# Kernel tuning notes

Measured on AMD Instinct MI355X. Metric: run time of the kernel, lower is better.

Reference implementation:

```python
import jax, jax.numpy as jnp
import numpy as np

H = 16          # nhead
N_LAYERS = 4    # stacks (weights are SHARED across stacks, as in the torch module)
PAD_IDX = 1
EPS = 1e-6
NEG = -1e9


def _pos_encoding(S, d):
    den = jnp.exp(-jnp.arange(0, d, 2, dtype=jnp.float32) * (np.log(10000.0) / d))
    ang = jnp.arange(S, dtype=jnp.float32)[:, None] * den[None, :]  # (S, d/2)
    pe = jnp.zeros((S, d), jnp.float32)
    pe = pe.at[:, 0::2].set(jnp.sin(ang)).at[:, 1::2].set(jnp.cos(ang))
    return pe


def _layer_norm(x, g, b):
    mu = jnp.mean(x, axis=-1, keepdims=True)
    var = jnp.mean((x - mu) ** 2, axis=-1, keepdims=True)
    return (x - mu) * jax.lax.rsqrt(var + EPS) * g + b


def _split_heads(x):
    B, S, d = x.shape
    return x.reshape(B, S, H, d // H).transpose(0, 2, 1, 3)  # (B,H,S,dk)


def _mha(q_in, k_in, v_in, mask, wq, bq, wk, bk, wv, bv, wo, bo):
    q = _split_heads(q_in @ wq + bq)
    k = _split_heads(k_in @ wk + bk)
    v = _split_heads(v_in @ wv + bv)
    dk = v.shape[-1]
    score = jnp.einsum('bhqd,bhkd->bhqk', q, k) / jnp.sqrt(jnp.float32(dk))
    if mask is not None:
        score = jnp.where(mask, score, NEG)
    p = jax.nn.softmax(score, axis=-1)
    out = jnp.einsum('bhqk,bhkd->bhqd', p, v)
    B, _, S, _ = out.shape
    out = out.transpose(0, 2, 1, 3).reshape(B, S, H * dk)
    return out @ wo + bo


def setup_inputs() -> dict:
    key = jax.random.key(0)
    B, St, Sm, d, dff, V = 4, 1024, 1024, 1024, 4096, 32000
    ks = jax.random.split(key, 32)
    sc = 1.0 / np.sqrt(d)
    inp = {
        'target_result': jax.random.randint(ks[0], (B, St), 0, V),
        'memory': jax.random.normal(ks[1], (B, Sm, d), jnp.float32),
        'emb': jax.random.normal(ks[2], (V, d), jnp.float32) * sc,
        'ff_w1': jax.random.normal(ks[3], (d, dff), jnp.float32) * sc,
        'ff_b1': jnp.zeros((dff,), jnp.float32),
        'ff_w2': jax.random.normal(ks[4], (dff, d), jnp.float32) / np.sqrt(dff),
        'ff_b2': jnp.zeros((d,), jnp.float32),
        'ln_g': jnp.ones((d,), jnp.float32),
        'ln_b': jnp.zeros((d,), jnp.float32),
    }
    i = 5
    for pre in ('sa', 'xa'):
        for nm in ('q', 'k', 'v', 'o'):
            inp[f'{pre}_w{nm}'] = jax.random.normal(ks[i], (d, d), jnp.float32) * sc
            inp[f'{pre}_b{nm}'] = jnp.zeros((d,), jnp.float32)
            i += 1
    return inp


def reference(target_result, memory, emb,
              sa_wq, sa_bq, sa_wk, sa_bk, sa_wv, sa_bv, sa_wo, sa_bo,
              xa_wq, xa_bq, xa_wk, xa_bk, xa_wv, xa_bv, xa_wo, xa_bo,
              ff_w1, ff_b1, ff_w2, ff_b2, ln_g, ln_b):
    B, St = target_result.shape
    d = emb.shape[1]
    # embed + scale + positional encoding (dropout = eval/identity)
    x = emb[target_result] * jnp.sqrt(jnp.float32(d)) + _pos_encoding(St, d)[None]
    # masks: pad mask (B,1,St,1) & causal (St,St) -> (B,1,St,St); source mask all-ones -> None
    pad = (target_result != PAD_IDX)[:, None, :, None]
    causal = jnp.tril(jnp.ones((St, St), bool))[None, None]
    tgt_mask = pad & causal
    out = x
    for _ in range(N_LAYERS):
        n = _layer_norm(out, ln_g, ln_b)
        out = out + _mha(n, n, n, tgt_mask,
                         sa_wq, sa_bq, sa_wk, sa_bk, sa_wv, sa_bv, sa_wo, sa_bo)
        n = _layer_norm(out, ln_g, ln_b)
        out = out + _mha(n, memory, memory, None,
                         xa_wq, xa_bq, xa_wk, xa_bk, xa_wv, xa_bv, xa_wo, xa_bo)
        n = _layer_norm(out, ln_g, ln_b)
        out = out + (jax.nn.relu(n @ ff_w1 + ff_b1) @ ff_w2 + ff_b2)
    return _layer_norm(out, ln_g, ln_b)
```

## Files before the change

kernel.cpp:

```cpp
#include <hip/hip_runtime.h>

typedef unsigned short u16;
typedef unsigned int u32;
typedef float f32x4 __attribute__((ext_vector_type(4)));
typedef float f32x16 __attribute__((ext_vector_type(16)));
typedef __bf16 bf16x8 __attribute__((ext_vector_type(8)));
typedef short short8 __attribute__((ext_vector_type(8)));
typedef u32 u32x4 __attribute__((ext_vector_type(4)));

#define DINLINE static __device__ __forceinline__

DINLINE u16 f2bf(float f) {
  u32 u = __builtin_bit_cast(u32, f);
  u += 0x7fffu + ((u >> 16) & 1u);
  return (u16)(u >> 16);
}

DINLINE float b2f(u32 lo16) {
  u32 u = lo16 << 16;
  return __builtin_bit_cast(float, u);
}

DINLINE f32x4 mfma16(short8 a, short8 b, f32x4 c) {
  return __builtin_amdgcn_mfma_f32_16x16x32_bf16(
      __builtin_bit_cast(bf16x8, a), __builtin_bit_cast(bf16x8, b), c, 0, 0, 0);
}

DINLINE f32x16 mfma32(short8 a, short8 b, f32x16 c) {
  return __builtin_amdgcn_mfma_f32_32x32x16_bf16(
      __builtin_bit_cast(bf16x8, a), __builtin_bit_cast(bf16x8, b), c, 0, 0, 0);
}

DINLINE u32 cvtpk(float lo, float hi) {
  u32 r;
  asm("v_cvt_pk_bf16_f32 %0, %1, %2" : "=v"(r) : "v"(lo), "v"(hi));
  return r;
}

DINLINE void plswap(u32& a, u32& b) {
  auto r = __builtin_amdgcn_permlane32_swap(a, b, false, false);
  a = (u32)r[0];
  b = (u32)r[1];
}

DINLINE void gld16(const void* g, void* l) {
  __builtin_amdgcn_global_load_lds(
      (const __attribute__((address_space(1))) void*)g,
      (__attribute__((address_space(3))) void*)l, 16, 0, 0);
}

__global__ __launch_bounds__(256) void transpose_wt(const float* __restrict__ src,
                                                    u16* __restrict__ dst, int K, int N,
                                                    float scale) {
  __shared__ float tile[32][33];
  int n0 = blockIdx.x * 32, k0 = blockIdx.y * 32;
  int tx = threadIdx.x, ty = threadIdx.y;
#pragma unroll
  for (int j = 0; j < 32; j += 8)
    tile[ty + j][tx] = src[(size_t)(k0 + ty + j) * N + n0 + tx];
  __syncthreads();
#pragma unroll
  for (int j = 0; j < 32; j += 8)
    dst[(size_t)(n0 + ty + j) * K + k0 + tx] = f2bf(tile[tx][ty + j] * scale);
}

__global__ __launch_bounds__(256) void cvt_bf16(const float* __restrict__ src,
                                                u16* __restrict__ dst) {
  size_t i = (size_t)blockIdx.x * 256 + threadIdx.x;
  float4 v = ((const float4*)src)[i];
  u32 lo = (u32)f2bf(v.x) | ((u32)f2bf(v.y) << 16);
  u32 hi = (u32)f2bf(v.z) | ((u32)f2bf(v.w) << 16);
  uint2 o; o.x = lo; o.y = hi;
  ((uint2*)dst)[i] = o;
}

__global__ void concat3(const float* __restrict__ a, const float* __restrict__ b,
                        const float* __restrict__ c, float* __restrict__ o, float sa) {
  int i = blockIdx.x * 256 + threadIdx.x;
  float v = (i < 1024) ? a[i] * sa : (i < 2048 ? b[i - 1024] : c[i - 2048]);
  o[i] = v;
}

__global__ void scale_vec(const float* __restrict__ a, float* __restrict__ o, float s) {
  int i = blockIdx.x * 256 + threadIdx.x;
  o[i] = a[i] * s;
}

__global__ __launch_bounds__(256) void pe_k(float* __restrict__ pe) {
  int s = blockIdx.x;
  for (int c = threadIdx.x; c < 1024; c += 256) {
    int i = c >> 1;
    float den = expf(-(float)(2 * i) * 0.0089944739960705f);
    float ang = (float)s * den;
    pe[s * 1024 + c] = (c & 1) ? cosf(ang) : sinf(ang);
  }
}

__global__ __launch_bounds__(256) void embed_pe(const int* __restrict__ tgt,
                                                const float* __restrict__ emb,
                                                const float* __restrict__ pe,
                                                float* __restrict__ x,
                                                u16* __restrict__ xbf) {
  int row = blockIdx.x;
  int s = row & 1023;
  int tok = tgt[row];
  float4 e = ((const float4*)(emb + (size_t)tok * 1024))[threadIdx.x];
  float4 p = ((const float4*)(pe + (size_t)s * 1024))[threadIdx.x];
  float4 o;
  o.x = e.x * 32.0f + p.x; o.y = e.y * 32.0f + p.y;
  o.z = e.z * 32.0f + p.z; o.w = e.w * 32.0f + p.w;
  ((float4*)(x + (size_t)row * 1024))[threadIdx.x] = o;
  ushort4 ob;
  ob.x = f2bf(o.x); ob.y = f2bf(o.y); ob.z = f2bf(o.z); ob.w = f2bf(o.w);
  ((ushort4*)(xbf + (size_t)row * 1024))[threadIdx.x] = ob;
}

template <int MODE>
__global__ __launch_bounds__(256) void ln2_k(const float* __restrict__ Xf,
                                             const u16* __restrict__ Xb,
                                             const float* __restrict__ g,
                                             const float* __restrict__ bta,
                                             u16* __restrict__ obf,
                                             float* __restrict__ of) {
  const int t = threadIdx.x;
  const int row = blockIdx.x * 2 + (t >> 7);
  const int c = t & 127;
  float v[8];
  if (MODE == 1) {
    float4 a = ((const float4*)(Xf + (size_t)row * 1024))[c * 2];
    float4 b4 = ((const float4*)(Xf + (size_t)row * 1024))[c * 2 + 1];
    v[0] = a.x; v[1] = a.y; v[2] = a.z; v[3] = a.w;
    v[4] = b4.x; v[5] = b4.y; v[6] = b4.z; v[7] = b4.w;
  } else {
    u32x4 p = *(const u32x4*)(Xb + (size_t)row * 1024 + c * 8);
#pragma unroll
    for (int i = 0; i < 4; ++i) {
      v[2 * i] = b2f(p[i]);
      v[2 * i + 1] = b2f(p[i] >> 16);
    }
  }
  float s = 0.f, sq = 0.f;
#pragma unroll
  for (int i = 0; i < 8; ++i) { s += v[i]; sq += v[i] * v[i]; }
#pragma unroll
  for (int o = 1; o < 64; o <<= 1) {
    s += __shfl_xor(s, o);
    sq += __shfl_xor(sq, o);
  }
  __shared__ float red[8];
  const int wid = t >> 6;
  if ((t & 63) == 0) { red[wid * 2] = s; red[wid * 2 + 1] = sq; }
  __syncthreads();
  const int base = (t >> 7) * 4;
  s = red[base] + red[base + 2];
  sq = red[base + 1] + red[base + 3];
  float mean = s * (1.0f / 1024.0f);
  float var = sq * (1.0f / 1024.0f) - mean * mean;
  float rstd = rsqrtf(var + 1e-6f);
  float4 g0 = ((const float4*)g)[c * 2], g1 = ((const float4*)g)[c * 2 + 1];
  float4 b0 = ((const float4*)bta)[c * 2], b1 = ((const float4*)bta)[c * 2 + 1];
  float gv[8] = {g0.x, g0.y, g0.z, g0.w, g1.x, g1.y, g1.z, g1.w};
  float bv[8] = {b0.x, b0.y, b0.z, b0.w, b1.x, b1.y, b1.z, b1.w};
  float y[8];
#pragma unroll
  for (int i = 0; i < 8; ++i) y[i] = (v[i] - mean) * rstd * gv[i] + bv[i];
  if (MODE == 1) {
    float4 o0, o1;
    o0.x = y[0]; o0.y = y[1]; o0.z = y[2]; o0.w = y[3];
    o1.x = y[4]; o1.y = y[5]; o1.z = y[6]; o1.w = y[7];
    ((float4*)(of + (size_t)row * 1024))[c * 2] = o0;
    ((float4*)(of + (size_t)row * 1024))[c * 2 + 1] = o1;
  } else {
    u32x4 o;
#pragma unroll
    for (int i = 0; i < 4; ++i)
      o[i] = (u32)f2bf(y[2 * i]) | ((u32)f2bf(y[2 * i + 1]) << 16);
    *(u32x4*)(obf + (size_t)row * 1024 + c * 8) = o;
  }
}

template <int BM, int EPI>
__global__ __launch_bounds__(256) void gemm2(
    const u16* __restrict__ A, const u16* __restrict__ Bt,
    const float* __restrict__ bias, float* __restrict__ X,
    u16* __restrict__ Cbf, int N, int K) {
  constexpr int ABYT = BM * 128;
  constexpr int BBYT = 128 * 128;
  constexpr int MF = BM / 32;
  __shared__ __align__(16) char smem[2 * (ABYT + BBYT)];

  const int tid = threadIdx.x;
  const int w = tid >> 6, l = tid & 63;
  const int lg = l >> 4, lc = l & 15;
  const int nwg = gridDim.x * gridDim.y;
  int bid = blockIdx.y * gridDim.x + blockIdx.x;
  bid = (bid & 7) * (nwg >> 3) + (bid >> 3);
  const int m0 = (bid / gridDim.x) * BM, n0 = (bid % gridDim.x) * 128;
  const int wr = w >> 1, wc = w & 1;
  const char* Ab = (const char*)A;
  const char* Bb = (const char*)Bt;
  const size_t sA = (size_t)K * 2;

  f32x4 acc[MF][4];
  const f32x4 zv = {0.f, 0.f, 0.f, 0.f};
#pragma unroll
  for (int m = 0; m < MF; ++m)
#pragma unroll
    for (int n = 0; n < 4; ++n) acc[m][n] = zv;

  const int srow = l >> 3;
  const int scol = ((l & 7) ^ srow) << 4;

  auto stage = [&](char* bufA, char* bufB, int kt) {
    const size_t kb = (size_t)kt << 7;
#pragma unroll
    for (int i = 0; i < BM / 32; ++i) {
      const int r = i * 32 + w * 8 + srow;
      gld16(Ab + (size_t)(m0 + r) * sA + kb + scol, bufA + (i * 4 + w) * 1024 + l * 16);
    }
#pragma unroll
    for (int i = 0; i < 4; ++i) {
      const int r = i * 32 + w * 8 + srow;
      gld16(Bb + (size_t)(n0 + r) * sA + kb + scol, bufB + (i * 4 + w) * 1024 + l * 16);
    }
  };

  stage(smem, smem + ABYT, 0);
  __syncthreads();

  const int nkt = K >> 6;
  int cur = 0;
  for (int kt = 0; kt < nkt; ++kt) {
    char* As = smem + cur * (ABYT + BBYT);
    char* Bs = As + ABYT;
    if (kt + 1 < nkt) {
      char* An = smem + (cur ^ 1) * (ABYT + BBYT);
      stage(An, An + ABYT, kt + 1);
    }
    __builtin_amdgcn_s_setprio(1);
#pragma unroll
    for (int ks = 0; ks < 2; ++ks) {
      short8 af[MF], bf4[4];
#pragma unroll
      for (int m = 0; m < MF; ++m) {
        int row = wr * (BM / 2) + m * 16 + lc;
        int col = (ks * 64 + (lg << 4)) ^ ((row & 7) << 4);
        af[m] = *(const short8*)(As + row * 128 + col);
      }
#pragma unroll
      for (int n = 0; n < 4; ++n) {
        int row = wc * 64 + n * 16 + lc;
        int col = (ks * 64 + (lg << 4)) ^ ((row & 7) << 4);
        bf4[n] = *(const short8*)(Bs + row * 128 + col);
      }
#pragma unroll
      for (int m = 0; m < MF; ++m)
#pragma unroll
        for (int n = 0; n < 4; ++n) acc[m][n] = mfma16(af[m], bf4[n], acc[m][n]);
    }
    __builtin_amdgcn_s_setprio(0);
    __syncthreads();
    cur ^= 1;
  }

  float bv[4];
#pragma unroll
  for (int n = 0; n < 4; ++n) bv[n] = bias[n0 + wc * 64 + n * 16 + lc];

  if (EPI <= 1) {
    u16* ct = (u16*)smem;
#pragma unroll
    for (int m = 0; m < MF; ++m)
#pragma unroll
      for (int n = 0; n < 4; ++n)
#pragma unroll
        for (int r = 0; r < 4; ++r) {
          int row = wr * (BM / 2) + m * 16 + (lg << 2) + r;
          int col = wc * 64 + n * 16 + lc;
          float v = acc[m][n][r] + bv[n];
          if (EPI == 1) v = v > 0.f ? v : 0.f;
          ct[row * 136 + col] = f2bf(v);
        }
    __syncthreads();
#pragma unroll
    for (int j = 0; j < BM / 16; ++j) {
      int c = j * 256 + tid;
      int row = c >> 4, colb = (c & 15) * 8;
      *(short8*)(Cbf + (size_t)(m0 + row) * N + n0 + colb) =
          *(const short8*)(ct + row * 136 + colb);
    }
  } else if (EPI == 2) {
    float* cf = (float*)smem;
#pragma unroll
    for (int m = 0; m < MF; ++m)
#pragma unroll
      for (int n = 0; n < 4; ++n)
#pragma unroll
        for (int r = 0; r < 4; ++r) {
          int row = wr * (BM / 2) + m * 16 + (lg << 2) + r;
          int col = wc * 64 + n * 16 + lc;
          cf[row * 128 + col] = acc[m][n][r] + bv[n];
        }
    __syncthreads();
#pragma unroll
    for (int j = 0; j < BM / 8; ++j) {
      int c = j * 256 + tid;
      int row = c >> 5, colb = (c & 31) * 4;
      size_t idx = (size_t)(m0 + row) * N + n0 + colb;
      float4 s4 = *(const float4*)(cf + row * 128 + colb);
      float4 xv = *(const float4*)(X + idx);
      xv.x += s4.x; xv.y += s4.y; xv.z += s4.z; xv.w += s4.w;
      *(float4*)(X + idx) = xv;
      ushort4 ob;
      ob.x = f2bf(xv.x); ob.y = f2bf(xv.y); ob.z = f2bf(xv.z); ob.w = f2bf(xv.w);
      *(ushort4*)(Cbf + idx) = ob;
    }
  } else {
    u16* ct = (u16*)smem;
#pragma unroll
    for (int m = 0; m < MF; ++m)
#pragma unroll
      for (int n = 0; n < 4; ++n)
#pragma unroll
        for (int r = 0; r < 4; ++r) {
          int row = wr * (BM / 2) + m * 16 + (lg << 2) + r;
          int col = wc * 64 + n * 16 + lc;
          ct[col * 136 + row] = f2bf(acc[m][n][r] + bv[n]);
        }
    __syncthreads();
    const int bb = m0 >> 10, ms = m0 & 1023;
#pragma unroll
    for (int j = 0; j < BM / 16; ++j) {
      int flat = j * 256 + tid;
      int sb = flat & (BM / 8 - 1);
      int col = flat / (BM / 8);
      int n = n0 + col;
      u16* dst = Cbf + (size_t)(((bb << 4) + (n >> 6)) * 64 + (n & 63)) * 1024 + ms + sb * 8;
      *(short8*)dst = *(const short8*)(ct + col * 136 + sb * 8);
    }
  }
}

template <int BM, int EPI>
__global__ __launch_bounds__(256) void gemm2c(
    const u16* __restrict__ A, const u16* __restrict__ Bt,
    const float* __restrict__ bias, float* __restrict__ X,
    u16* __restrict__ Cbf, int N, int K) {
  constexpr int ABYT = BM * 128;
  constexpr int BBYT = 128 * 128;
  constexpr int BUF = ABYT + BBYT;
  constexpr int MF = BM / 32;
  __shared__ __align__(16) char smem[3 * BUF];

  const int tid = threadIdx.x;
  const int w = tid >> 6, l = tid & 63;
  const int lg = l >> 4, lc = l & 15;
  const int nwg = gridDim.x * gridDim.y;
  int bid = blockIdx.y * gridDim.x + blockIdx.x;
  bid = (bid & 7) * (nwg >> 3) + (bid >> 3);
  const int m0 = (bid / gridDim.x) * BM, n0 = (bid % gridDim.x) * 128;
  const int wr = w >> 1, wc = w & 1;
  const char* Ab = (const char*)A;
  const char* Bb = (const char*)Bt;
  const size_t sA = (size_t)K * 2;

  f32x4 acc[MF][4];
  const f32x4 zv = {0.f, 0.f, 0.f, 0.f};
#pragma unroll
  for (int m = 0; m < MF; ++m)
#pragma unroll
    for (int n = 0; n < 4; ++n) acc[m][n] = zv;

  const int srow = l >> 3;
  const int scol = ((l & 7) ^ srow) << 4;

  auto stage = [&](char* buf, int kt) {
    const size_t kb = (size_t)kt << 7;
#pragma unroll
    for (int i = 0; i < BM / 32; ++i) {
      const int r = i * 32 + w * 8 + srow;
      gld16(Ab + (size_t)(m0 + r) * sA + kb + scol, buf + (i * 4 + w) * 1024 + l * 16);
    }
#pragma unroll
    for (int i = 0; i < 4; ++i) {
      const int r = i * 32 + w * 8 + srow;
      gld16(Bb + (size_t)(n0 + r) * sA + kb + scol,
            buf + ABYT + (i * 4 + w) * 1024 + l * 16);
    }
  };

  char* p0 = smem;
  char* p1 = smem + BUF;
  char* p2 = smem + 2 * BUF;

  stage(p0, 0);
  stage(p1, 1);
  __builtin_amdgcn_sched_barrier(0);
  asm volatile("s_waitcnt vmcnt(6)" ::: "memory");
  __builtin_amdgcn_s_barrier();
  __builtin_amdgcn_sched_barrier(0);

  const int nkt = K >> 6;
  for (int kt = 0; kt < nkt; ++kt) {
    if (kt + 2 < nkt) stage(p2, kt + 2);
    const char* As = p0;
    const char* Bs = p0 + ABYT;
    __builtin_amdgcn_s_setprio(1);
#pragma unroll
    for (int ks = 0; ks < 2; ++ks) {
      short8 af[MF], bf4[4];
#pragma unroll
      for (int m = 0; m < MF; ++m) {
        int row = wr * (BM / 2) + m * 16 + lc;
        int col = (ks * 64 + (lg << 4)) ^ ((row & 7) << 4);
        af[m] = *(const short8*)(As + row * 128 + col);
      }
#pragma unroll
      for (int n = 0; n < 4; ++n) {
        int row = wc * 64 + n * 16 + lc;
        int col = (ks * 64 + (lg << 4)) ^ ((row & 7) << 4);
        bf4[n] = *(const short8*)(Bs + row * 128 + col);
      }
#pragma unroll
      for (int m = 0; m < MF; ++m)
#pragma unroll
        for (int n = 0; n < 4; ++n) acc[m][n] = mfma16(af[m], bf4[n], acc[m][n]);
    }
    __builtin_amdgcn_s_setprio(0);
    __builtin_amdgcn_sched_barrier(0);
    if (kt + 2 < nkt) {
      asm volatile("s_waitcnt vmcnt(6) lgkmcnt(0)" ::: "memory");
    } else {
      asm volatile("s_waitcnt vmcnt(0) lgkmcnt(0)" ::: "memory");
    }
    __builtin_amdgcn_s_barrier();
    __builtin_amdgcn_sched_barrier(0);
    char* t = p0; p0 = p1; p1 = p2; p2 = t;
  }

  float bv[4];
#pragma unroll
  for (int n = 0; n < 4; ++n) bv[n] = bias[n0 + wc * 64 + n * 16 + lc];

  if (EPI <= 1) {
    u16* ct = (u16*)smem;
#pragma unroll
    for (int m = 0; m < MF; ++m)
#pragma unroll
      for (int n = 0; n < 4; ++n)
#pragma unroll
        for (int r = 0; r < 4; ++r) {
          int row = wr * (BM / 2) + m * 16 + (lg << 2) + r;
          int col = wc * 64 + n * 16 + lc;
          float v = acc[m][n][r] + bv[n];
          if (EPI == 1) v = v > 0.f ? v : 0.f;
          ct[row * 136 + col] = f2bf(v);
        }
    __syncthreads();
#pragma unroll
    for (int j = 0; j < BM / 16; ++j) {
      int c = j * 256 + tid;
      int row = c >> 4, colb = (c & 15) * 8;
      *(short8*)(Cbf + (size_t)(m0 + row) * N + n0 + colb) =
          *(const short8*)(ct + row * 136 + colb);
    }
  } else if (EPI == 2) {
    float* cf = (float*)smem;
#pragma unroll
    for (int m = 0; m < MF; ++m)
#pragma unroll
      for (int n = 0; n < 4; ++n)
#pragma unroll
        for (int r = 0; r < 4; ++r) {
          int row = wr * (BM / 2) + m * 16 + (lg << 2) + r;
          int col = wc * 64 + n * 16 + lc;
          cf[row * 128 + col] = acc[m][n][r] + bv[n];
        }
    __syncthreads();
#pragma unroll
    for (int j = 0; j < BM / 8; ++j) {
      int c = j * 256 + tid;
      int row = c >> 5, colb = (c & 31) * 4;
      size_t idx = (size_t)(m0 + row) * N + n0 + colb;
      float4 s4 = *(const float4*)(cf + row * 128 + colb);
      float4 xv = *(const float4*)(X + idx);
      xv.x += s4.x; xv.y += s4.y; xv.z += s4.z; xv.w += s4.w;
      *(float4*)(X + idx) = xv;
      ushort4 ob;
      ob.x = f2bf(xv.x); ob.y = f2bf(xv.y); ob.z = f2bf(xv.z); ob.w = f2bf(xv.w);
      *(ushort4*)(Cbf + idx) = ob;
    }
  } else {
    u16* ct = (u16*)smem;
#pragma unroll
    for (int m = 0; m < MF; ++m)
#pragma unroll
      for (int n = 0; n < 4; ++n)
#pragma unroll
        for (int r = 0; r < 4; ++r) {
          int row = wr * (BM / 2) + m * 16 + (lg << 2) + r;
          int col = wc * 64 + n * 16 + lc;
          ct[col * 136 + row] = f2bf(acc[m][n][r] + bv[n]);
        }
    __syncthreads();
    const int bb = m0 >> 10, ms = m0 & 1023;
#pragma unroll
    for (int j = 0; j < BM / 16; ++j) {
      int flat = j * 256 + tid;
      int sb = flat & (BM / 8 - 1);
      int col = flat / (BM / 8);
      int n = n0 + col;
      u16* dst = Cbf + (size_t)(((bb << 4) + (n >> 6)) * 64 + (n & 63)) * 1024 + ms + sb * 8;
      *(short8*)dst = *(const short8*)(ct + col * 136 + sb * 8);
    }
  }
}

template <bool CAUSAL>
__global__ __launch_bounds__(256) void attn_lds(
    const u16* __restrict__ Qp, int sQ, const u16* __restrict__ Kp, int sK,
    const u16* __restrict__ Vt, const int* __restrict__ tgt,
    u16* __restrict__ Out) {
  __shared__ __align__(16) char smem[2][32768];
  const int tid = threadIdx.x;
  const int w = tid >> 6, l = tid & 63;
  const int bh = blockIdx.x & 63;
  const int p = blockIdx.x >> 6;
  const int sub = CAUSAL ? ((p < 4) ? p : 11 - p) : p;
  const int b = bh >> 4, h = bh & 15;
  const int lq = l & 31, hi = l >> 5;
  const int qt = sub * 4 + w;
  const int q0 = qt * 32;

  const char* Kc = (const char*)(Kp + (size_t)b * 1024 * sK + h * 64);
  const char* Vc = (const char*)(Vt + (size_t)bh * 64 * 1024);
  const u16* Qh = Qp + (size_t)b * 1024 * sQ + h * 64;

  short8 qb[4];
  {
    const u16* qrow = Qh + (size_t)(q0 + lq) * sQ + hi * 8;
#pragma unroll
    for (int c = 0; c < 4; ++c) qb[c] = *(const short8*)(qrow + c * 16);
  }

  bool row_ok = true;
  int my_nkt = 16;
  int blk_nst = CAUSAL ? (sub + 1) : 8;
  if (CAUSAL) {
    row_ok = (tgt[b * 1024 + q0 + lq] != 1);
    bool anypad_w = __any(!row_ok);
    __shared__ int s_pad;
    if (tid == 0) s_pad = 0;
    __syncthreads();
    if (anypad_w && l == 0) s_pad = 1;
    __syncthreads();
    if (s_pad) { my_nkt = 16; blk_nst = 8; }
    else my_nkt = (qt >> 1) + 1;
  }

  const int srow = l >> 3;
  const int scol = ((l & 7) ^ srow) << 4;
  auto stage = [&](int buf, int st) {
    const int k0 = st * 128;
    char* Ks = smem[buf];
    char* Vs = smem[buf] + 16384;
#pragma unroll
    for (int t2 = 0; t2 < 2; ++t2)
#pragma unroll
      for (int i = 0; i < 2; ++i) {
        const int r = i * 32 + w * 8 + srow;
        gld16(Kc + (size_t)(k0 + t2 * 64 + r) * sK * 2 + scol, Ks + t2 * 8192 + r * 128);
        gld16(Vc + (size_t)r * 2048 + (size_t)(k0 + t2 * 64) * 2 + scol,
              Vs + t2 * 8192 + r * 128);
      }
  };

  float m = -3.0e38f, lsum = 0.f;
  f32x16 oacc[2];
#pragma unroll
  for (int r = 0; r < 16; ++r) { oacc[0][r] = 0.f; oacc[1][r] = 0.f; }

  stage(0, 0);
  __syncthreads();
  int cur = 0;

  for (int st = 0; st < blk_nst; ++st) {
    if (st + 1 < blk_nst) stage(cur ^ 1, st + 1);
#pragma unroll
    for (int t2 = 0; t2 < 2; ++t2) {
      const int t64 = st * 2 + t2;
      if (t64 < my_nkt) {
        const char* Ks = smem[cur] + t2 * 8192;
        const char* Vs = smem[cur] + 16384 + t2 * 8192;
        const int k0 = t64 * 64;
        f32x16 stt[2];
        __builtin_amdgcn_s_setprio(1);
#pragma unroll
        for (int s = 0; s < 2; ++s) {
          const int row = s * 32 + lq;
          const int swz = (row & 7) << 4;
          f32x16 a;
#pragma unroll
          for (int r = 0; r < 16; ++r) a[r] = 0.f;
#pragma unroll
          for (int c = 0; c < 4; ++c) {
            short8 kb = *(const short8*)(Ks + row * 128 + ((c * 32 + hi * 16) ^ swz));
            a = mfma32(kb, qb[c], a);
          }
          stt[s] = a;
        }
        __builtin_amdgcn_s_setprio(0);
        if (CAUSAL) {
#pragma unroll
          for (int s = 0; s < 2; ++s) {
            if (!row_ok || (k0 + s * 32 + 31 > q0)) {
#pragma unroll
              for (int r = 0; r < 16; ++r) {
                int kg = k0 + s * 32 + (r & 3) + 8 * (r >> 2) + 4 * hi;
                bool ok = row_ok && (kg <= q0 + lq);
                if (!ok) stt[s][r] = -1e9f;
              }
            }
          }
        }
        float tm;
        {
          float v[16];
#pragma unroll
          for (int r = 0; r < 16; ++r) v[r] = fmaxf(stt[0][r], stt[1][r]);
#pragma unroll
          for (int w2 = 8; w2 >= 1; w2 >>= 1)
#pragma unroll
            for (int r = 0; r < w2; ++r) v[r] = fmaxf(v[r], v[r + w2]);
          tm = v[0];
        }
        tm = fmaxf(tm, __shfl_xor(tm, 32));
        if (!__all(tm <= m + 8.0f)) {
          float mn = fmaxf(m, tm);
          float alpha = __expf(m - mn);
          lsum *= alpha;
          m = mn;
#pragma unroll
          for (int r = 0; r < 16; ++r) {
            int crow = (r & 3) + 8 * (r >> 2) + 4 * hi;
            float av = __shfl(alpha, crow);
            oacc[0][r] *= av;
            oacc[1][r] *= av;
          }
        }
        float tsa0 = 0.f, tsa1 = 0.f, tsa2 = 0.f, tsa3 = 0.f;
#pragma unroll
        for (int s = 0; s < 2; ++s) {
#pragma unroll
          for (int r = 0; r < 16; ++r) {
            float e = __expf(stt[s][r] - m);
            stt[s][r] = e;
            if ((r & 3) == 0) tsa0 += e;
            else if ((r & 3) == 1) tsa1 += e;
            else if ((r & 3) == 2) tsa2 += e;
            else tsa3 += e;
          }
        }
        float ts = (tsa0 + tsa1) + (tsa2 + tsa3);
        ts += __shfl_xor(ts, 32);
        lsum += ts;
        short8 pa[4];
#pragma unroll
        for (int s = 0; s < 2; ++s) {
          u32 cc[8];
#pragma unroll
          for (int t = 0; t < 4; ++t) {
            cc[2 * t]     = cvtpk(stt[s][4 * t + 0], stt[s][4 * t + 1]);
            cc[2 * t + 1] = cvtpk(stt[s][4 * t + 2], stt[s][4 * t + 3]);
          }
          plswap(cc[0], cc[2]);
          plswap(cc[1], cc[3]);
          plswap(cc[4], cc[6]);
          plswap(cc[5], cc[7]);
          u32x4 w0 = {cc[0], cc[1], cc[2], cc[3]};
          u32x4 w1 = {cc[4], cc[5], cc[6], cc[7]};
          pa[2 * s]     = __builtin_bit_cast(short8, w0);
          pa[2 * s + 1] = __builtin_bit_cast(short8, w1);
        }
        __builtin_amdgcn_s_setprio(1);
#pragma unroll
        for (int dt = 0; dt < 2; ++dt) {
          const int row = dt * 32 + lq;
          const int swz = (row & 7) << 4;
#pragma unroll
          for (int c = 0; c < 4; ++c) {
            short8 vb = *(const short8*)(Vs + row * 128 + ((c * 32 + hi * 16) ^ swz));
            oacc[dt] = mfma32(pa[c], vb, oacc[dt]);
          }
        }
        __builtin_amdgcn_s_setprio(0);
      }
    }
    __syncthreads();
    cur ^= 1;
  }

#pragma unroll
  for (int r = 0; r < 16; ++r) {
    int crow = (r & 3) + 8 * (r >> 2) + 4 * hi;
    float lv = __shfl(lsum, crow);
    float linv = 1.0f / lv;
    int qg = q0 + crow;
    size_t base = ((size_t)b * 1024 + qg) * 1024 + h * 64 + lq;
    Out[base] = f2bf(oacc[0][r] * linv);
    Out[base + 32] = f2bf(oacc[1][r] * linv);
  }
}

extern "C" void kernel_launch(void* const* d_in, const int* in_sizes, int n_in,
                              void* d_out, int out_size, void* d_ws, size_t ws_size,
                              hipStream_t stream) {
  const int* tgt = (const int*)d_in[0];
  const float* memory = (const float*)d_in[1];
  const float* emb = (const float*)d_in[2];
  const float* ff_w1 = (const float*)d_in[3];
  const float* ff_b1 = (const float*)d_in[4];
  const float* ff_w2 = (const float*)d_in[5];
  const float* ff_b2 = (const float*)d_in[6];
  const float* ln_g = (const float*)d_in[7];
  const float* ln_b = (const float*)d_in[8];
  const float* sa_wq = (const float*)d_in[9];
  const float* sa_bq = (const float*)d_in[10];
  const float* sa_wk = (const float*)d_in[11];
  const float* sa_bk = (const float*)d_in[12];
  const float* sa_wv = (const float*)d_in[13];
  const float* sa_bv = (const float*)d_in[14];
  const float* sa_wo = (const float*)d_in[15];
  const float* sa_bo = (const float*)d_in[16];
  const float* xa_wq = (const float*)d_in[17];
  const float* xa_bq = (const float*)d_in[18];
  const float* xa_wk = (const float*)d_in[19];
  const float* xa_bk = (const float*)d_in[20];
  const float* xa_wv = (const float*)d_in[21];
  const float* xa_bv = (const float*)d_in[22];
  const float* xa_wo = (const float*)d_in[23];
  const float* xa_bo = (const float*)d_in[24];

  char* ws = (char*)d_ws;
  size_t off = 0;
  auto alloc = [&](size_t bytes) {
    char* p = ws + off;
    off += (bytes + 255) & ~(size_t)255;
    return p;
  };
  float* x   = (float*)alloc(4096ull * 1024 * 4);
  u16* xbf   = (u16*)alloc(4096ull * 1024 * 2);
  u16* nbf   = (u16*)alloc(4096ull * 1024 * 2);
  u16* qkv   = (u16*)alloc(4096ull * 2048 * 2);
  u16* q2    = (u16*)alloc(4096ull * 1024 * 2);
  u16* attn  = (u16*)alloc(4096ull * 1024 * 2);
  u16* vt    = (u16*)alloc(64ull * 64 * 1024 * 2);
  u16* kx    = (u16*)alloc(4096ull * 1024 * 2);
  u16* vtx   = (u16*)alloc(64ull * 64 * 1024 * 2);
  u16* h1    = (u16*)alloc(4096ull * 4096 * 2);
  u16* memb  = (u16*)alloc(4096ull * 1024 * 2);
  u16* w_qkv = (u16*)alloc(3072ull * 1024 * 2);
  u16* w_sao = (u16*)alloc(1024ull * 1024 * 2);
  u16* w_xaq = (u16*)alloc(1024ull * 1024 * 2);
  u16* w_xak = (u16*)alloc(1024ull * 1024 * 2);
  u16* w_xav = (u16*)alloc(1024ull * 1024 * 2);
  u16* w_xao = (u16*)alloc(1024ull * 1024 * 2);
  u16* w_ff1 = (u16*)alloc(4096ull * 1024 * 2);
  u16* w_ff2 = (u16*)alloc(1024ull * 4096 * 2);
  float* b_qkv = (float*)alloc(3072 * 4);
  float* b_xaq = (float*)alloc(1024 * 4);
  float* pe    = (float*)alloc(1024ull * 1024 * 4);

  dim3 blk(256);
  dim3 b32(32, 8);
  const float QS = 0.125f;

  transpose_wt<<<dim3(32, 32), b32, 0, stream>>>(sa_wq, w_qkv, 1024, 1024, QS);
  transpose_wt<<<dim3(32, 32), b32, 0, stream>>>(sa_wk, w_qkv + 1024 * 1024, 1024, 1024, 1.f);
  transpose_wt<<<dim3(32, 32), b32, 0, stream>>>(sa_wv, w_qkv + 2048 * 1024, 1024, 1024, 1.f);
  transpose_wt<<<dim3(32, 32), b32, 0, stream>>>(sa_wo, w_sao, 1024, 1024, 1.f);
  transpose_wt<<<dim3(32, 32), b32, 0, stream>>>(xa_wq, w_xaq, 1024, 1024, QS);
  transpose_wt<<<dim3(32, 32), b32, 0, stream>>>(xa_wk, w_xak, 1024, 1024, 1.f);
  transpose_wt<<<dim3(32, 32), b32, 0, stream>>>(xa_wv, w_xav, 1024, 1024, 1.f);
  transpose_wt<<<dim3(32, 32), b32, 0, stream>>>(xa_wo, w_xao, 1024, 1024, 1.f);
  transpose_wt<<<dim3(128, 32), b32, 0, stream>>>(ff_w1, w_ff1, 1024, 4096, 1.f);
  transpose_wt<<<dim3(32, 128), b32, 0, stream>>>(ff_w2, w_ff2, 4096, 1024, 1.f);
  concat3<<<12, blk, 0, stream>>>(sa_bq, sa_bk, sa_bv, b_qkv, QS);
  scale_vec<<<4, blk, 0, stream>>>(xa_bq, b_xaq, QS);
  cvt_bf16<<<4096, blk, 0, stream>>>(memory, memb);
  pe_k<<<1024, blk, 0, stream>>>(pe);
  embed_pe<<<4096, blk, 0, stream>>>(tgt, emb, pe, x, xbf);

  gemm2c<64, 0><<<dim3(8, 64), blk, 0, stream>>>(memb, w_xak, xa_bk, nullptr, kx, 1024, 1024);
  gemm2c<64, 3><<<dim3(8, 64), blk, 0, stream>>>(memb, w_xav, xa_bv, nullptr, vtx, 1024, 1024);

  for (int layer = 0; layer < 4; ++layer) {
    ln2_k<2><<<2048, blk, 0, stream>>>(nullptr, xbf, ln_g, ln_b, nbf, nullptr);
    gemm2<128, 0><<<dim3(16, 32), blk, 0, stream>>>(nbf, w_qkv, b_qkv, nullptr, qkv, 2048, 1024);
    gemm2c<64, 3><<<dim3(8, 64), blk, 0, stream>>>(nbf, w_qkv + 2048 * 1024, b_qkv + 2048,
                                                   nullptr, vt, 1024, 1024);
    attn_lds<true><<<512, blk, 0, stream>>>(qkv, 2048, qkv + 1024, 2048, vt, tgt, attn);
    gemm2c<64, 2><<<dim3(8, 64), blk, 0, stream>>>(attn, w_sao, sa_bo, x, xbf, 1024, 1024);
    ln2_k<2><<<2048, blk, 0, stream>>>(nullptr, xbf, ln_g, ln_b, nbf, nullptr);
    gemm2c<64, 0><<<dim3(8, 64), blk, 0, stream>>>(nbf, w_xaq, b_xaq, nullptr, q2, 1024, 1024);
    attn_lds<false><<<512, blk, 0, stream>>>(q2, 1024, kx, 1024, vtx, nullptr, attn);
    gemm2c<64, 2><<<dim3(8, 64), blk, 0, stream>>>(attn, w_xao, xa_bo, x, xbf, 1024, 1024);
    ln2_k<2><<<2048, blk, 0, stream>>>(nullptr, xbf, ln_g, ln_b, nbf, nullptr);
    gemm2<128, 1><<<dim3(32, 32), blk, 0, stream>>>(nbf, w_ff1, ff_b1, nullptr, h1, 4096, 1024);
    gemm2c<64, 2><<<dim3(8, 64), blk, 0, stream>>>(h1, w_ff2, ff_b2, x, xbf, 1024, 4096);
  }
  ln2_k<1><<<2048, blk, 0, stream>>>(x, nullptr, ln_g, ln_b, nullptr, (float*)d_out);
}
```

Measured before the change: 1.082 ms.

## Fold LayerNorm into GEMMs via gamma-scaled weights and epilogue row-stat correction

Removes the standalone LayerNorm kernels inside the layer loop. Gamma is folded into the transposed weights, and the beta and bias terms go into precomputed column vectors u and c. The consumer GEMMs read the raw bf16 residual and apply per-row rstd and mean corrections in the epilogue. The residual-add GEMM epilogues (and the embedding kernel) write per-tile partial row sums and sums of squares, which the next GEMM reduces into the row statistics. This saves a full read/write pass of the activations three times per layer, at the cost of extra epilogue work. It also changes numerics: the mean-subtraction now happens after a bf16 matmul on the uncentred input (E[x²]-μ² cancellation), and the statistics come from fp32 values rather than the bf16 copy.

```diff
diff --git a/kernel.cpp b/kernel.cpp
--- a/kernel.cpp
+++ b/kernel.cpp
@@ -62,6 +62,39 @@
 #pragma unroll
   for (int j = 0; j < 32; j += 8)
     dst[(size_t)(n0 + ty + j) * K + k0 + tx] = f2bf(tile[tx][ty + j] * scale);
+}
+
+__global__ __launch_bounds__(256) void transpose_wtg(const float* __restrict__ src,
+                                                     u16* __restrict__ dst, int K, int N,
+                                                     float scale, const float* __restrict__ g) {
+  __shared__ float tile[32][33];
+  int n0 = blockIdx.x * 32, k0 = blockIdx.y * 32;
+  int tx = threadIdx.x, ty = threadIdx.y;
+#pragma unroll
+  for (int j = 0; j < 32; j += 8)
+    tile[ty + j][tx] = src[(size_t)(k0 + ty + j) * N + n0 + tx];
+  __syncthreads();
+  float gk = g[k0 + tx] * scale;
+#pragma unroll
+  for (int j = 0; j < 32; j += 8)
+    dst[(size_t)(n0 + ty + j) * K + k0 + tx] = f2bf(tile[tx][ty + j] * gk);
+}
+
+__global__ __launch_bounds__(256) void ucol_k(const float* __restrict__ g,
+                                              const float* __restrict__ bln,
+                                              const float* __restrict__ W,
+                                              const float* __restrict__ bias,
+                                              float scale, int N,
+                                              float* __restrict__ u, float* __restrict__ c) {
+  int n = blockIdx.x * 256 + threadIdx.x;
+  float us = 0.f, cs = 0.f;
+  for (int k = 0; k < 1024; ++k) {
+    float wv = W[(size_t)k * N + n];
+    us += g[k] * wv;
+    cs += bln[k] * wv;
+  }
+  u[n] = scale * us;
+  c[n] = scale * (cs + bias[n]);
 }
 
 __global__ __launch_bounds__(256) void cvt_bf16(const float* __restrict__ src,
@@ -74,18 +107,6 @@
   ((uint2*)dst)[i] = o;
 }
 
-__global__ void concat3(const float* __restrict__ a, const float* __restrict__ b,
-                        const float* __restrict__ c, float* __restrict__ o, float sa) {
-  int i = blockIdx.x * 256 + threadIdx.x;
-  float v = (i < 1024) ? a[i] * sa : (i < 2048 ? b[i - 1024] : c[i - 2048]);
-  o[i] = v;
-}
-
-__global__ void scale_vec(const float* __restrict__ a, float* __restrict__ o, float s) {
-  int i = blockIdx.x * 256 + threadIdx.x;
-  o[i] = a[i] * s;
-}
-
 __global__ __launch_bounds__(256) void pe_k(float* __restrict__ pe) {
   int s = blockIdx.x;
   for (int c = threadIdx.x; c < 1024; c += 256) {
@@ -100,45 +121,55 @@
                                                 const float* __restrict__ emb,
                                                 const float* __restrict__ pe,
                                                 float* __restrict__ x,
-                                                u16* __restrict__ xbf) {
+                                                u16* __restrict__ xbf,
+                                                float2* __restrict__ pstat) {
   int row = blockIdx.x;
   int s = row & 1023;
   int tok = tgt[row];
-  float4 e = ((const float4*)(emb + (size_t)tok * 1024))[threadIdx.x];
-  float4 p = ((const float4*)(pe + (size_t)s * 1024))[threadIdx.x];
+  int t = threadIdx.x;
+  float4 e = ((const float4*)(emb + (size_t)tok * 1024))[t];
+  float4 p = ((const float4*)(pe + (size_t)s * 1024))[t];
   float4 o;
   o.x = e.x * 32.0f + p.x; o.y = e.y * 32.0f + p.y;
   o.z = e.z * 32.0f + p.z; o.w = e.w * 32.0f + p.w;
-  ((float4*)(x + (size_t)row * 1024))[threadIdx.x] = o;
+  ((float4*)(x + (size_t)row * 1024))[t] = o;
   ushort4 ob;
   ob.x = f2bf(o.x); ob.y = f2bf(o.y); ob.z = f2bf(o.z); ob.w = f2bf(o.w);
-  ((ushort4*)(xbf + (size_t)row * 1024))[threadIdx.x] = ob;
-}
-
-template <int MODE>
-__global__ __launch_bounds__(256) void ln2_k(const float* __restrict__ Xf,
-                                             const u16* __restrict__ Xb,
-                                             const float* __restrict__ g,
-                                             const float* __restrict__ bta,
-                                             u16* __restrict__ obf,
-                                             float* __restrict__ of) {
+  ((ushort4*)(xbf + (size_t)row * 1024))[t] = ob;
+  float sm = o.x + o.y + o.z + o.w;
+  float sq = o.x * o.x + o.y * o.y + o.z * o.z + o.w * o.w;
+#pragma unroll
+  for (int w2 = 1; w2 < 64; w2 <<= 1) {
+    sm += __shfl_xor(sm, w2);
+    sq += __shfl_xor(sq, w2);
+  }
+  __shared__ float red[8];
+  int wid = t >> 6;
+  if ((t & 63) == 0) { red[wid * 2] = sm; red[wid * 2 + 1] = sq; }
+  __syncthreads();
+  if (t == 0) {
+    float2 st;
+    st.x = red[0] + red[2] + red[4] + red[6];
+    st.y = red[1] + red[3] + red[5] + red[7];
+    pstat[row] = st;
+  } else if (t < 8) {
+    float2 z; z.x = 0.f; z.y = 0.f;
+    pstat[t * 4096 + row] = z;
+  }
+}
+
+__global__ __launch_bounds__(256) void ln_fin(const float* __restrict__ Xf,
+                                              const float* __restrict__ g,
+                                              const float* __restrict__ bta,
+                                              float* __restrict__ of) {
   const int t = threadIdx.x;
   const int row = blockIdx.x * 2 + (t >> 7);
   const int c = t & 127;
   float v[8];
-  if (MODE == 1) {
-    float4 a = ((const float4*)(Xf + (size_t)row * 1024))[c * 2];
-    float4 b4 = ((const float4*)(Xf + (size_t)row * 1024))[c * 2 + 1];
-    v[0] = a.x; v[1] = a.y; v[2] = a.z; v[3] = a.w;
-    v[4] = b4.x; v[5] = b4.y; v[6] = b4.z; v[7] = b4.w;
-  } else {
-    u32x4 p = *(const u32x4*)(Xb + (size_t)row * 1024 + c * 8);
-#pragma unroll
-    for (int i = 0; i < 4; ++i) {
-      v[2 * i] = b2f(p[i]);
-      v[2 * i + 1] = b2f(p[i] >> 16);
-    }
-  }
+  float4 a = ((const float4*)(Xf + (size_t)row * 1024))[c * 2];
+  float4 b4 = ((const float4*)(Xf + (size_t)row * 1024))[c * 2 + 1];
+  v[0] = a.x; v[1] = a.y; v[2] = a.z; v[3] = a.w;
+  v[4] = b4.x; v[5] = b4.y; v[6] = b4.z; v[7] = b4.w;
   float s = 0.f, sq = 0.f;
 #pragma unroll
   for (int i = 0; i < 8; ++i) { s += v[i]; sq += v[i] * v[i]; }
@@ -161,33 +192,30 @@
   float4 b0 = ((const float4*)bta)[c * 2], b1 = ((const float4*)bta)[c * 2 + 1];
   float gv[8] = {g0.x, g0.y, g0.z, g0.w, g1.x, g1.y, g1.z, g1.w};
   float bv[8] = {b0.x, b0.y, b0.z, b0.w, b1.x, b1.y, b1.z, b1.w};
-  float y[8];
-#pragma unroll
-  for (int i = 0; i < 8; ++i) y[i] = (v[i] - mean) * rstd * gv[i] + bv[i];
-  if (MODE == 1) {
-    float4 o0, o1;
-    o0.x = y[0]; o0.y = y[1]; o0.z = y[2]; o0.w = y[3];
-    o1.x = y[4]; o1.y = y[5]; o1.z = y[6]; o1.w = y[7];
-    ((float4*)(of + (size_t)row * 1024))[c * 2] = o0;
-    ((float4*)(of + (size_t)row * 1024))[c * 2 + 1] = o1;
-  } else {
-    u32x4 o;
-#pragma unroll
-    for (int i = 0; i < 4; ++i)
-      o[i] = (u32)f2bf(y[2 * i]) | ((u32)f2bf(y[2 * i + 1]) << 16);
-    *(u32x4*)(obf + (size_t)row * 1024 + c * 8) = o;
-  }
+  float4 o0, o1;
+  o0.x = (v[0] - mean) * rstd * gv[0] + bv[0];
+  o0.y = (v[1] - mean) * rstd * gv[1] + bv[1];
+  o0.z = (v[2] - mean) * rstd * gv[2] + bv[2];
+  o0.w = (v[3] - mean) * rstd * gv[3] + bv[3];
+  o1.x = (v[4] - mean) * rstd * gv[4] + bv[4];
+  o1.y = (v[5] - mean) * rstd * gv[5] + bv[5];
+  o1.z = (v[6] - mean) * rstd * gv[6] + bv[6];
+  o1.w = (v[7] - mean) * rstd * gv[7] + bv[7];
+  ((float4*)(of + (size_t)row * 1024))[c * 2] = o0;
+  ((float4*)(of + (size_t)row * 1024))[c * 2 + 1] = o1;
 }
 
 template <int BM, int EPI>
 __global__ __launch_bounds__(256) void gemm2(
     const u16* __restrict__ A, const u16* __restrict__ Bt,
     const float* __restrict__ bias, float* __restrict__ X,
-    u16* __restrict__ Cbf, int N, int K) {
+    u16* __restrict__ Cbf, const float* __restrict__ u, const float* __restrict__ cc,
+    const float2* __restrict__ pin, float2* __restrict__ pout, int N, int K) {
   constexpr int ABYT = BM * 128;
   constexpr int BBYT = 128 * 128;
   constexpr int MF = BM / 32;
   __shared__ __align__(16) char smem[2 * (ABYT + BBYT)];
+  __shared__ float s_rs[BM], s_mr[BM];
 
   const int tid = threadIdx.x;
   const int w = tid >> 6, l = tid & 63;
@@ -263,11 +291,32 @@
     cur ^= 1;
   }
 
-  float bv[4];
-#pragma unroll
-  for (int n = 0; n < 4; ++n) bv[n] = bias[n0 + wc * 64 + n * 16 + lc];
-
-  if (EPI <= 1) {
+  if (EPI >= 4) {
+    if (tid < BM) {
+      float s = 0.f, sq = 0.f;
+#pragma unroll
+      for (int sl = 0; sl < 8; ++sl) {
+        float2 p = pin[sl * 4096 + m0 + tid];
+        s += p.x; sq += p.y;
+      }
+      float mu = s * (1.0f / 1024.0f);
+      float var = sq * (1.0f / 1024.0f) - mu * mu;
+      float rs = rsqrtf(var + 1e-6f);
+      s_rs[tid] = rs;
+      s_mr[tid] = -mu * rs;
+    }
+    __syncthreads();
+  }
+
+  float bv[4], uv[4];
+#pragma unroll
+  for (int n = 0; n < 4; ++n) {
+    int col = n0 + wc * 64 + n * 16 + lc;
+    bv[n] = (EPI >= 4) ? cc[col] : bias[col];
+    uv[n] = (EPI >= 4) ? u[col] : 0.f;
+  }
+
+  if (EPI == 0 || EPI == 1 || EPI == 4 || EPI == 5) {
     u16* ct = (u16*)smem;
 #pragma unroll
     for (int m = 0; m < MF; ++m)
@@ -275,11 +324,13 @@
       for (int n = 0; n < 4; ++n)
 #pragma unroll
         for (int r = 0; r < 4; ++r) {
-          int row = wr * (BM / 2) + m * 16 + (lg << 2) + r;
+          int lr = wr * (BM / 2) + m * 16 + (lg << 2) + r;
           int col = wc * 64 + n * 16 + lc;
-          float v = acc[m][n][r] + bv[n];
-          if (EPI == 1) v = v > 0.f ? v : 0.f;
-          ct[row * 136 + col] = f2bf(v);
+          float v;
+          if (EPI >= 4) v = s_rs[lr] * acc[m][n][r] + s_mr[lr] * uv[n] + bv[n];
+          else v = acc[m][n][r] + bv[n];
+          if (EPI == 1 || EPI == 5) v = v > 0.f ? v : 0.f;
+          ct[lr * 136 + col] = f2bf(v);
         }
     __syncthreads();
 #pragma unroll
@@ -314,6 +365,20 @@
       ushort4 ob;
       ob.x = f2bf(xv.x); ob.y = f2bf(xv.y); ob.z = f2bf(xv.z); ob.w = f2bf(xv.w);
       *(ushort4*)(Cbf + idx) = ob;
+      *(float4*)(cf + row * 128 + colb) = xv;
+    }
+    __syncthreads();
+    if (tid < BM) {
+      float s = 0.f, sq = 0.f;
+      const float4* rowp = (const float4*)(cf + tid * 128);
+#pragma unroll
+      for (int i2 = 0; i2 < 32; ++i2) {
+        float4 q4 = rowp[i2];
+        s += q4.x + q4.y + q4.z + q4.w;
+        sq += q4.x * q4.x + q4.y * q4.y + q4.z * q4.z + q4.w * q4.w;
+      }
+      float2 st; st.x = s; st.y = sq;
+      pout[(n0 >> 7) * 4096 + m0 + tid] = st;
     }
   } else {
     u16* ct = (u16*)smem;
@@ -323,9 +388,12 @@
       for (int n = 0; n < 4; ++n)
 #pragma unroll
         for (int r = 0; r < 4; ++r) {
-          int row = wr * (BM / 2) + m * 16 + (lg << 2) + r;
+          int lr = wr * (BM / 2) + m * 16 + (lg << 2) + r;
           int col = wc * 64 + n * 16 + lc;
-          ct[col * 136 + row] = f2bf(acc[m][n][r] + bv[n]);
+          float v;
+          if (EPI >= 4) v = s_rs[lr] * acc[m][n][r] + s_mr[lr] * uv[n] + bv[n];
+          else v = acc[m][n][r] + bv[n];
+          ct[col * 136 + lr] = f2bf(v);
         }
     __syncthreads();
     const int bb = m0 >> 10, ms = m0 & 1023;
@@ -345,12 +413,14 @@
 __global__ __launch_bounds__(256) void gemm2c(
     const u16* __restrict__ A, const u16* __restrict__ Bt,
     const float* __restrict__ bias, float* __restrict__ X,
-    u16* __restrict__ Cbf, int N, int K) {
+    u16* __restrict__ Cbf, const float* __restrict__ u, const float* __restrict__ cc,
+    const float2* __restrict__ pin, float2* __restrict__ pout, int N, int K) {
   constexpr int ABYT = BM * 128;
   constexpr int BBYT = 128 * 128;
   constexpr int BUF = ABYT + BBYT;
   constexpr int MF = BM / 32;
   __shared__ __align__(16) char smem[3 * BUF];
+  __shared__ float s_rs[BM], s_mr[BM];
 
   const int tid = threadIdx.x;
   const int w = tid >> 6, l = tid & 63;
@@ -438,11 +508,32 @@
     char* t = p0; p0 = p1; p1 = p2; p2 = t;
   }
 
-  float bv[4];
-#pragma unroll
-  for (int n = 0; n < 4; ++n) bv[n] = bias[n0 + wc * 64 + n * 16 + lc];
-
-  if (EPI <= 1) {
+  if (EPI >= 4) {
+    if (tid < BM) {
+      float s = 0.f, sq = 0.f;
+#pragma unroll
+      for (int sl = 0; sl < 8; ++sl) {
+        float2 p = pin[sl * 4096 + m0 + tid];
+        s += p.x; sq += p.y;
+      }
+      float mu = s * (1.0f / 1024.0f);
+      float var = sq * (1.0f / 1024.0f) - mu * mu;
+      float rs = rsqrtf(var + 1e-6f);
+      s_rs[tid] = rs;
+      s_mr[tid] = -mu * rs;
+    }
+    __syncthreads();
+  }
+
+  float bv[4], uv[4];
+#pragma unroll
+  for (int n = 0; n < 4; ++n) {
+    int col = n0 + wc * 64 + n * 16 + lc;
+    bv[n] = (EPI >= 4) ? cc[col] : bias[col];
+    uv[n] = (EPI >= 4) ? u[col] : 0.f;
+  }
+
+  if (EPI == 0 || EPI == 1 || EPI == 4 || EPI == 5) {
     u16* ct = (u16*)smem;
 #pragma unroll
     for (int m = 0; m < MF; ++m)
@@ -450,11 +541,13 @@
       for (int n = 0; n < 4; ++n)
 #pragma unroll
         for (int r = 0; r < 4; ++r) {
-          int row = wr * (BM / 2) + m * 16 + (lg << 2) + r;
+          int lr = wr * (BM / 2) + m * 16 + (lg << 2) + r;
           int col = wc * 64 + n * 16 + lc;
-          float v = acc[m][n][r] + bv[n];
-          if (EPI == 1) v = v > 0.f ? v : 0.f;
-          ct[row * 136 + col] = f2bf(v);
+          float v;
+          if (EPI >= 4) v = s_rs[lr] * acc[m][n][r] + s_mr[lr] * uv[n] + bv[n];
+          else v = acc[m][n][r] + bv[n];
+          if (EPI == 1 || EPI == 5) v = v > 0.f ? v : 0.f;
+          ct[lr * 136 + col] = f2bf(v);
         }
     __syncthreads();
 #pragma unroll
@@ -489,6 +582,20 @@
       ushort4 ob;
       ob.x = f2bf(xv.x); ob.y = f2bf(xv.y); ob.z = f2bf(xv.z); ob.w = f2bf(xv.w);
       *(ushort4*)(Cbf + idx) = ob;
+      *(float4*)(cf + row * 128 + colb) = xv;
+    }
+    __syncthreads();
+    if (tid < BM) {
+      float s = 0.f, sq = 0.f;
+      const float4* rowp = (const float4*)(cf + tid * 128);
+#pragma unroll
+      for (int i2 = 0; i2 < 32; ++i2) {
+        float4 q4 = rowp[i2];
+        s += q4.x + q4.y + q4.z + q4.w;
+        sq += q4.x * q4.x + q4.y * q4.y + q4.z * q4.z + q4.w * q4.w;
+      }
+      float2 st; st.x = s; st.y = sq;
+      pout[(n0 >> 7) * 4096 + m0 + tid] = st;
     }
   } else {
     u16* ct = (u16*)smem;
@@ -498,9 +605,12 @@
       for (int n = 0; n < 4; ++n)
 #pragma unroll
         for (int r = 0; r < 4; ++r) {
-          int row = wr * (BM / 2) + m * 16 + (lg << 2) + r;
+          int lr = wr * (BM / 2) + m * 16 + (lg << 2) + r;
           int col = wc * 64 + n * 16 + lc;
-          ct[col * 136 + row] = f2bf(acc[m][n][r] + bv[n]);
+          float v;
+          if (EPI >= 4) v = s_rs[lr] * acc[m][n][r] + s_mr[lr] * uv[n] + bv[n];
+          else v = acc[m][n][r] + bv[n];
+          ct[col * 136 + lr] = f2bf(v);
         }
     __syncthreads();
     const int bb = m0 >> 10, ms = m0 & 1023;
@@ -667,18 +777,18 @@
         short8 pa[4];
 #pragma unroll
         for (int s = 0; s < 2; ++s) {
-          u32 cc[8];
+          u32 cc2[8];
 #pragma unroll
           for (int t = 0; t < 4; ++t) {
-            cc[2 * t]     = cvtpk(stt[s][4 * t + 0], stt[s][4 * t + 1]);
-            cc[2 * t + 1] = cvtpk(stt[s][4 * t + 2], stt[s][4 * t + 3]);
+            cc2[2 * t]     = cvtpk(stt[s][4 * t + 0], stt[s][4 * t + 1]);
+            cc2[2 * t + 1] = cvtpk(stt[s][4 * t + 2], stt[s][4 * t + 3]);
           }
-          plswap(cc[0], cc[2]);
-          plswap(cc[1], cc[3]);
-          plswap(cc[4], cc[6]);
-          plswap(cc[5], cc[7]);
-          u32x4 w0 = {cc[0], cc[1], cc[2], cc[3]};
-          u32x4 w1 = {cc[4], cc[5], cc[6], cc[7]};
+          plswap(cc2[0], cc2[2]);
+          plswap(cc2[1], cc2[3]);
+          plswap(cc2[4], cc2[6]);
+          plswap(cc2[5], cc2[7]);
+          u32x4 w0 = {cc2[0], cc2[1], cc2[2], cc2[3]};
+          u32x4 w1 = {cc2[4], cc2[5], cc2[6], cc2[7]};
           pa[2 * s]     = __builtin_bit_cast(short8, w0);
           pa[2 * s + 1] = __builtin_bit_cast(short8, w1);
         }
@@ -750,7 +860,6 @@
   };
   float* x   = (float*)alloc(4096ull * 1024 * 4);
   u16* xbf   = (u16*)alloc(4096ull * 1024 * 2);
-  u16* nbf   = (u16*)alloc(4096ull * 1024 * 2);
   u16* qkv   = (u16*)alloc(4096ull * 2048 * 2);
   u16* q2    = (u16*)alloc(4096ull * 1024 * 2);
   u16* attn  = (u16*)alloc(4096ull * 1024 * 2);
@@ -767,47 +876,61 @@
   u16* w_xao = (u16*)alloc(1024ull * 1024 * 2);
   u16* w_ff1 = (u16*)alloc(4096ull * 1024 * 2);
   u16* w_ff2 = (u16*)alloc(1024ull * 4096 * 2);
-  float* b_qkv = (float*)alloc(3072 * 4);
-  float* b_xaq = (float*)alloc(1024 * 4);
+  float* u_qkv = (float*)alloc(3072 * 4);
+  float* c_qkv = (float*)alloc(3072 * 4);
+  float* u_xaq = (float*)alloc(1024 * 4);
+  float* c_xaq = (float*)alloc(1024 * 4);
+  float* u_ff1 = (float*)alloc(4096 * 4);
+  float* c_ff1 = (float*)alloc(4096 * 4);
+  float2* pstat = (float2*)alloc(8ull * 4096 * 8);
   float* pe    = (float*)alloc(1024ull * 1024 * 4);
 
   dim3 blk(256);
   dim3 b32(32, 8);
   const float QS = 0.125f;
 
-  transpose_wt<<<dim3(32, 32), b32, 0, stream>>>(sa_wq, w_qkv, 1024, 1024, QS);
-  transpose_wt<<<dim3(32, 32), b32, 0, stream>>>(sa_wk, w_qkv + 1024 * 1024, 1024, 1024, 1.f);
-  transpose_wt<<<dim3(32, 32), b32, 0, stream>>>(sa_wv, w_qkv + 2048 * 1024, 1024, 1024, 1.f);
+  transpose_wtg<<<dim3(32, 32), b32, 0, stream>>>(sa_wq, w_qkv, 1024, 1024, QS, ln_g);
+  transpose_wtg<<<dim3(32, 32), b32, 0, stream>>>(sa_wk, w_qkv + 1024 * 1024, 1024, 1024, 1.f, ln_g);
+  transpose_wtg<<<dim3(32, 32), b32, 0, stream>>>(sa_wv, w_qkv + 2048 * 1024, 1024, 1024, 1.f, ln_g);
   transpose_wt<<<dim3(32, 32), b32, 0, stream>>>(sa_wo, w_sao, 1024, 1024, 1.f);
-  transpose_wt<<<dim3(32, 32), b32, 0, stream>>>(xa_wq, w_xaq, 1024, 1024, QS);
+  transpose_wtg<<<dim3(32, 32), b32, 0, stream>>>(xa_wq, w_xaq, 1024, 1024, QS, ln_g);
   transpose_wt<<<dim3(32, 32), b32, 0, stream>>>(xa_wk, w_xak, 1024, 1024, 1.f);
   transpose_wt<<<dim3(32, 32), b32, 0, stream>>>(xa_wv, w_xav, 1024, 1024, 1.f);
   transpose_wt<<<dim3(32, 32), b32, 0, stream>>>(xa_wo, w_xao, 1024, 1024, 1.f);
-  transpose_wt<<<dim3(128, 32), b32, 0, stream>>>(ff_w1, w_ff1, 1024, 4096, 1.f);
+  transpose_wtg<<<dim3(128, 32), b32, 0, stream>>>(ff_w1, w_ff1, 1024, 4096, 1.f, ln_g);
   transpose_wt<<<dim3(32, 128), b32, 0, stream>>>(ff_w2, w_ff2, 4096, 1024, 1.f);
-  concat3<<<12, blk, 0, stream>>>(sa_bq, sa_bk, sa_bv, b_qkv, QS);
-  scale_vec<<<4, blk, 0, stream>>>(xa_bq, b_xaq, QS);
+  ucol_k<<<4, blk, 0, stream>>>(ln_g, ln_b, sa_wq, sa_bq, QS, 1024, u_qkv, c_qkv);
+  ucol_k<<<4, blk, 0, stream>>>(ln_g, ln_b, sa_wk, sa_bk, 1.f, 1024, u_qkv + 1024, c_qkv + 1024);
+  ucol_k<<<4, blk, 0, stream>>>(ln_g, ln_b, sa_wv, sa_bv, 1.f, 1024, u_qkv + 2048, c_qkv + 2048);
+  ucol_k<<<4, blk, 0, stream>>>(ln_g, ln_b, xa_wq, xa_bq, QS, 1024, u_xaq, c_xaq);
+  ucol_k<<<16, blk, 0, stream>>>(ln_g, ln_b, ff_w1, ff_b1, 1.f, 4096, u_ff1, c_ff1);
   cvt_bf16<<<4096, blk, 0, stream>>>(memory, memb);
   pe_k<<<1024, blk, 0, stream>>>(pe);
-  embed_pe<<<4096, blk, 0, stream>>>(tgt, emb, pe, x, xbf);
-
-  gemm2c<64, 0><<<dim3(8, 64), blk, 0, stream>>>(memb, w_xak, xa_bk, nullptr, kx, 1024, 1024);
-  gemm2c<64, 3><<<dim3(8, 64), blk, 0, stream>>>(memb, w_xav, xa_bv, nullptr, vtx, 1024, 1024);
+  embed_pe<<<4096, blk, 0, stream>>>(tgt, emb, pe, x, xbf, pstat);
+
+  gemm2c<64, 0><<<dim3(8, 64), blk, 0, stream>>>(memb, w_xak, xa_bk, nullptr, kx,
+                                                 nullptr, nullptr, nullptr, nullptr, 1024, 1024);
+  gemm2c<64, 3><<<dim3(8, 64), blk, 0, stream>>>(memb, w_xav, xa_bv, nullptr, vtx,
+                                                 nullptr, nullptr, nullptr, nullptr, 1024, 1024);
 
   for (int layer = 0; layer < 4; ++layer) {
-    ln2_k<2><<<2048, blk, 0, stream>>>(nullptr, xbf, ln_g, ln_b, nbf, nullptr);
-    gemm2<128, 0><<<dim3(16, 32), blk, 0, stream>>>(nbf, w_qkv, b_qkv, nullptr, qkv, 2048, 1024);
-    gemm2c<64, 3><<<dim3(8, 64), blk, 0, stream>>>(nbf, w_qkv + 2048 * 1024, b_qkv + 2048,
-                                                   nullptr, vt, 1024, 1024);
+    gemm2<128, 4><<<dim3(16, 32), blk, 0, stream>>>(xbf, w_qkv, nullptr, nullptr, qkv,
+                                                    u_qkv, c_qkv, pstat, nullptr, 2048, 1024);
+    gemm2c<64, 6><<<dim3(8, 64), blk, 0, stream>>>(xbf, w_qkv + 2048 * 1024, nullptr, nullptr, vt,
+                                                   u_qkv + 2048, c_qkv + 2048, pstat, nullptr,
+                                                   1024, 1024);
     attn_lds<true><<<512, blk, 0, stream>>>(qkv, 2048, qkv + 1024, 2048, vt, tgt, attn);
-    gemm2c<64, 2><<<dim3(8, 64), blk, 0, stream>>>(attn, w_sao, sa_bo, x, xbf, 1024, 1024);
-    ln2_k<2><<<2048, blk, 0, stream>>>(nullptr, xbf, ln_g, ln_b, nbf, nullptr);
-    gemm2c<64, 0><<<dim3(8, 64), blk, 0, stream>>>(nbf, w_xaq, b_xaq, nullptr, q2, 1024, 1024);
+    gemm2c<64, 2><<<dim3(8, 64), blk, 0, stream>>>(attn, w_sao, sa_bo, x, xbf,
+                                                   nullptr, nullptr, nullptr, pstat, 1024, 1024);
+    gemm2c<64, 4><<<dim3(8, 64), blk, 0, stream>>>(xbf, w_xaq, nullptr, nullptr, q2,
+                                                   u_xaq, c_xaq, pstat, nullptr, 1024, 1024);
     attn_lds<false><<<512, blk, 0, stream>>>(q2, 1024, kx, 1024, vtx, nullptr, attn);
-    gemm2c<64, 2><<<dim3(8, 64), blk, 0, stream>>>(attn, w_xao, xa_bo, x, xbf, 1024, 1024);
-    ln2_k<2><<<2048, blk, 0, stream>>>(nullptr, xbf, ln_g, ln_b, nbf, nullptr);
-    gemm2<128, 1><<<dim3(32, 32), blk, 0, stream>>>(nbf, w_ff1, ff_b1, nullptr, h1, 4096, 1024);
-    gemm2c<64, 2><<<dim3(8, 64), blk, 0, stream>>>(h1, w_ff2, ff_b2, x, xbf, 1024, 4096);
-  }
-  ln2_k<1><<<2048, blk, 0, stream>>>(x, nullptr, ln_g, ln_b, nullptr, (float*)d_out);
-}
+    gemm2c<64, 2><<<dim3(8, 64), blk, 0, stream>>>(attn, w_xao, xa_bo, x, xbf,
+                                                   nullptr, nullptr, nullptr, pstat, 1024, 1024);
+    gemm2<128, 5><<<dim3(32, 32), blk, 0, stream>>>(xbf, w_ff1, nullptr, nullptr, h1,
+                                                    u_ff1, c_ff1, pstat, nullptr, 4096, 1024);
+    gemm2c<64, 2><<<dim3(8, 64), blk, 0, stream>>>(h1, w_ff2, ff_b2, x, xbf,
+                                                   nullptr, nullptr, nullptr, pstat, 1024, 4096);
+  }
+  ln_fin<<<2048, blk, 0, stream>>>(x, ln_g, ln_b, (float*)d_out);
+}
```

Result: slower. 1.522 ms (+40.7%).
